# Kernel optimization log

Measured on AMD Instinct MI355X. Metric: run time of the kernel, lower is better.

Reference implementation:

```python
import jax, jax.numpy as jnp
import numpy as np

DIM = 512
H = 8
HD = DIM // H  # head_dim = 64


def setup_inputs() -> dict:
    key = jax.random.key(0)
    k1, k2, k3 = jax.random.split(key, 3)
    B, N = 16, 4096
    x = jax.random.normal(k1, (B, DIM, N), jnp.float32)
    # qkv_proj: Conv1d(dim, H*(1+2*HD), kernel=1) == linear over channels
    Wqkv = jax.random.normal(k2, (H * (1 + 2 * HD), DIM), jnp.float32) * 0.02
    bqkv = jnp.zeros((H * (1 + 2 * HD),), jnp.float32)
    # proj: Conv1d(dim, dim, kernel=1)
    Wp = jax.random.normal(k3, (DIM, DIM), jnp.float32) * 0.02
    bp = jnp.zeros((DIM,), jnp.float32)
    return {"x": x, "Wqkv": Wqkv, "bqkv": bqkv, "Wp": Wp, "bp": bp}


def reference(x, Wqkv, bqkv, Wp, bp):
    B, C, N = x.shape
    # 1x1 conv projection -> [B, H*(1+2*HD), N]
    qkv = jnp.einsum('oc,bcn->bon', Wqkv, x) + bqkv[None, :, None]
    qkv = qkv.reshape(B, H, 1 + 2 * HD, N)
    q = qkv[:, :, 0:1, :]          # [B,H,1,N]
    k = qkv[:, :, 1:1 + HD, :]     # [B,H,HD,N]
    v = qkv[:, :, 1 + HD:, :]      # [B,H,HD,N]
    scores = jax.nn.softmax(q, axis=-1)              # softmax over N
    ctx = jnp.sum(k * scores, axis=-1, keepdims=True)  # [B,H,HD,1]
    out = jax.nn.relu(v) * ctx                         # [B,H,HD,N]
    # permute/split/cat in torch == [B,H,HD,N] -> [B,N,H*HD] -> [B,C,N]
    out = out.transpose(0, 3, 1, 2).reshape(B, N, H * HD)
    out = out.transpose(0, 2, 1)                       # [B,C,N]
    out = jnp.einsum('oc,bcn->bon', Wp, out) + bp[None, :, None]
    return out
```

## Files before the change

### kernel.cpp

```cpp
#include <hip/hip_runtime.h>

#define NB 16
#define NC 512
#define NN 4096
#define NH 8

typedef __attribute__((ext_vector_type(8))) __bf16 bf16x8;
typedef __attribute__((ext_vector_type(4))) float f32x4;

__device__ __forceinline__ unsigned short f2bf(float f) {
    union { float f; unsigned u; } x; x.f = f;
    unsigned r = x.u + 0x7FFF + ((x.u >> 16) & 1);
    return (unsigned short)(r >> 16);
}

__global__ void pack_kernel(const float* __restrict__ Wqkv, const float* __restrict__ bqkv,
                            const float* __restrict__ Wp,
                            unsigned short* __restrict__ Wv_bf, unsigned short* __restrict__ Wp_bf,
                            float* __restrict__ bv) {
    int t = blockIdx.x * 256 + threadIdx.x;
    int j = t >> 9, c = t & 511;
    int h = j >> 6, d = j & 63;
    Wv_bf[t] = f2bf(Wqkv[((size_t)h * 129 + 65 + d) * 512 + c]);
    Wp_bf[t] = f2bf(Wp[t]);
    if (t < 512) bv[t] = bqkv[(t >> 6) * 129 + 65 + (t & 63)];
}

__global__ __launch_bounds__(256) void q_kernel(
        const float* __restrict__ x, const float* __restrict__ Wqkv,
        float* __restrict__ qP) {
    __shared__ float Ws[8][64];
    int n0 = blockIdx.x * 512, c0 = blockIdx.y * 64, b = blockIdx.z;
    int t = threadIdx.x;
    for (int i = t; i < 512; i += 256)
        Ws[i >> 6][i & 63] = Wqkv[(size_t)(i >> 6) * (129 * 512) + c0 + (i & 63)];
    __syncthreads();

    float acc[8][2];
#pragma unroll
    for (int h = 0; h < 8; h++) { acc[h][0] = 0.f; acc[h][1] = 0.f; }

    const float* xb = x + ((size_t)b * NC + c0) * NN + n0;
#pragma unroll 4
    for (int c = 0; c < 64; c++) {
        float2 v = *((const float2*)(xb + (size_t)c * NN) + t);
#pragma unroll
        for (int h = 0; h < 8; h++) {
            float w = Ws[h][c];
            acc[h][0] += w * v.x;
            acc[h][1] += w * v.y;
        }
    }
#pragma unroll
    for (int h = 0; h < 8; h++) {
        float2 o; o.x = acc[h][0]; o.y = acc[h][1];
        *((float2*)(qP + ((size_t)(blockIdx.y * NB + b) * 8 + h) * NN + n0) + t) = o;
    }
}

__global__ void softmax_kernel(const float* __restrict__ qP, float* __restrict__ sT) {
    int bh = blockIdx.x;
    int b = bh >> 3, h = bh & 7;
    int t = threadIdx.x;
    __shared__ float red[8];
    const float* qp = qP + (size_t)bh * NN;
    const size_t cstr = (size_t)NB * 8 * NN;
    float v[16];
    float mx = -1e30f;
#pragma unroll
    for (int i = 0; i < 16; i++) {
        int n = t + i * 256;
        float s = 0.f;
#pragma unroll
        for (int cb = 0; cb < 8; cb++) s += qp[cb * cstr + n];
        v[i] = s; mx = fmaxf(mx, s);
    }
#pragma unroll
    for (int o = 32; o; o >>= 1) mx = fmaxf(mx, __shfl_xor(mx, o));
    if ((t & 63) == 0) red[t >> 6] = mx;
    __syncthreads();
    mx = fmaxf(fmaxf(red[0], red[1]), fmaxf(red[2], red[3]));
    float s = 0.f;
#pragma unroll
    for (int i = 0; i < 16; i++) { v[i] = __expf(v[i] - mx); s += v[i]; }
#pragma unroll
    for (int o = 32; o; o >>= 1) s += __shfl_xor(s, o);
    __syncthreads();
    if ((t & 63) == 0) red[4 + (t >> 6)] = s;
    __syncthreads();
    float inv = 1.f / (red[4] + red[5] + red[6] + red[7]);
#pragma unroll
    for (int i = 0; i < 16; i++) {
        int n = t + i * 256;
        sT[((size_t)b * NN + n) * 8 + h] = v[i] * inv;
    }
}

__global__ __launch_bounds__(256) void xbar_kernel(
        const float* __restrict__ x, const float* __restrict__ sT,
        float* __restrict__ xbarP) {
    __shared__ float red[4][8][64];
    int c0 = blockIdx.x * 32, sl = blockIdx.y, b = blockIdx.z;
    int t = threadIdx.x;
    int l = t & 63, w = t >> 6;
    int nsl0 = sl * 512;
    float s_[8][8];
    {
        const f32x4* sp = (const f32x4*)(sT + ((size_t)b * NN + nsl0 + l * 8) * 8);
#pragma unroll
        for (int j = 0; j < 8; j++) {
            f32x4 a = sp[2 * j], bq = sp[2 * j + 1];
            s_[j][0] = a[0]; s_[j][1] = a[1]; s_[j][2] = a[2]; s_[j][3] = a[3];
            s_[j][4] = bq[0]; s_[j][5] = bq[1]; s_[j][6] = bq[2]; s_[j][7] = bq[3];
        }
    }
    float acc[8][8];
#pragma unroll
    for (int r = 0; r < 8; r++)
#pragma unroll
        for (int h = 0; h < 8; h++) acc[r][h] = 0.f;

    const float* xr = x + ((size_t)b * NC + c0 + w * 8) * NN + nsl0 + l * 8;
#pragma unroll
    for (int r = 0; r < 8; r++) {
        float4 a0 = *(const float4*)(xr + (size_t)r * NN);
        float4 a1 = *(const float4*)(xr + (size_t)r * NN + 4);
        float xf[8] = {a0.x, a0.y, a0.z, a0.w, a1.x, a1.y, a1.z, a1.w};
#pragma unroll
        for (int j = 0; j < 8; j++)
#pragma unroll
            for (int h = 0; h < 8; h++) acc[r][h] += xf[j] * s_[j][h];
    }
#pragma unroll
    for (int r = 0; r < 8; r++)
#pragma unroll
        for (int h = 0; h < 8; h++) {
            float a = acc[r][h];
            a += __shfl_xor(a, 8);
            a += __shfl_xor(a, 16);
            a += __shfl_xor(a, 32);
            acc[r][h] = a;
        }
    if (l < 8) {
#pragma unroll
        for (int r = 0; r < 8; r++)
#pragma unroll
            for (int h = 0; h < 8; h++) red[w][l][r * 8 + h] = acc[r][h];
    }
    __syncthreads();
    {
        int idx = t & 63;
        float v = 0.f;
#pragma unroll
        for (int res = 0; res < 8; res++) v += red[w][res][idx];
        int r = idx >> 3, h = idx & 7;
        xbarP[(((size_t)sl * NB + b) * 8 + h) * NC + c0 + w * 8 + r] = v;
    }
}

__global__ void ctx_kernel(const float* __restrict__ xbarP, const float* __restrict__ Wqkv,
                           const float* __restrict__ bqkv, float* __restrict__ ctx) {
    int bh = blockIdx.x; int b = bh >> 3, h = bh & 7;
    int t = threadIdx.x;
    __shared__ float xb[512];
    for (int i = t; i < 512; i += 256) {
        float s = 0.f;
#pragma unroll
        for (int sl = 0; sl < 8; sl++) s += xbarP[(((size_t)sl * NB + b) * 8 + h) * NC + i];
        xb[i] = s;
    }
    __syncthreads();
    int d = t >> 2, sub = t & 3;
    const float* wk = Wqkv + ((size_t)h * 129 + 1 + d) * 512;
    float acc = 0.f;
    for (int i = sub * 4; i < 512; i += 16) {
        float4 w = *(const float4*)(wk + i);
        acc += w.x * xb[i] + w.y * xb[i + 1] + w.z * xb[i + 2] + w.w * xb[i + 3];
    }
    acc += __shfl_xor(acc, 1);
    acc += __shfl_xor(acc, 2);
    if (sub == 0) ctx[(size_t)b * NC + h * 64 + d] = acc + bqkv[h * 129 + 1 + d];
}

__global__ __launch_bounds__(512, 2) void fused_gemm_kernel(
    const unsigned short* __restrict__ Wv,
    const unsigned short* __restrict__ Wp,
    const float* __restrict__ x,
    const float* __restrict__ bv,
    const float* __restrict__ bp,
    const float* __restrict__ ctx,
    float* __restrict__ outp)
{
    __shared__ alignas(16) unsigned short Ms[16 * 128 * 32];
    __shared__ alignas(16) unsigned short Bs[128 * 32];
    int b = blockIdx.y, n0 = blockIdx.x * 128;
    int t = threadIdx.x;
    int lane = t & 63, wid = t >> 6;
    int wj = wid >> 1, wn = wid & 1;
    int g = lane >> 4, col = lane & 15;
    int koff = g * 8;

    int sc = t >> 4, sn8 = (t & 15) * 8;

    f32x4 acc[8][4];
#pragma unroll
    for (int i = 0; i < 8; i++)
#pragma unroll
        for (int j = 0; j < 4; j++) { f32x4 z = {0.f, 0.f, 0.f, 0.f}; acc[i][j] = z; }

    bf16x8 afc[8], afn[8];
#pragma unroll
    for (int i = 0; i < 8; i++)
        afc[i] = *(const bf16x8*)(Wv + (size_t)(wj * 128 + i * 16 + col) * 512 + koff);

#pragma unroll 2
    for (int ks = 0; ks < 16; ks++) {
        int kk = ks * 32;
        {
            const float* xr = x + ((size_t)b * NC + kk + sc) * NN + n0 + sn8;
            float4 v0 = *(const float4*)(xr);
            float4 v1 = *(const float4*)(xr + 4);
            unsigned short xv[8] = {f2bf(v0.x), f2bf(v0.y), f2bf(v0.z), f2bf(v0.w),
                                    f2bf(v1.x), f2bf(v1.y), f2bf(v1.z), f2bf(v1.w)};
#pragma unroll
            for (int i = 0; i < 8; i++) {
                int nl = sn8 + i;
                int byte = nl * 64 + ((sc * 2) ^ (((nl >> 3) & 3) << 4));
                *(unsigned short*)((char*)Bs + byte) = xv[i];
            }
        }
        if (ks < 15) {
#pragma unroll
            for (int i = 0; i < 8; i++)
                afn[i] = *(const bf16x8*)(Wv + (size_t)(wj * 128 + i * 16 + col) * 512 + kk + 32 + koff);
        }
        __syncthreads();
        bf16x8 bfr[4];
#pragma unroll
        for (int j = 0; j < 4; j++) {
            int row = wn * 64 + j * 16 + col;
            int byte = row * 64 + ((koff * 2) ^ (((row >> 3) & 3) << 4));
            bfr[j] = *(const bf16x8*)((const char*)Bs + byte);
        }
#pragma unroll
        for (int i = 0; i < 8; i++)
#pragma unroll
            for (int j = 0; j < 4; j++)
                acc[i][j] = __builtin_amdgcn_mfma_f32_16x16x32_bf16(afc[i], bfr[j], acc[i][j], 0, 0, 0);
        __syncthreads();
#pragma unroll
        for (int i = 0; i < 8; i++) afc[i] = afn[i];
    }

#pragma unroll
    for (int i = 0; i < 8; i++) {
        int j0 = wj * 128 + i * 16 + g * 4;
        float4 bv4 = *(const float4*)(bv + j0);
        float4 cx4 = *(const float4*)(ctx + (size_t)b * NC + j0);
#pragma unroll
        for (int j = 0; j < 4; j++) {
            int n = wn * 64 + j * 16 + col;
            f32x4 a = acc[i][j];
            unsigned short h0 = f2bf(fmaxf(a[0] + bv4.x, 0.f) * cx4.x);
            unsigned short h1 = f2bf(fmaxf(a[1] + bv4.y, 0.f) * cx4.y);
            unsigned short h2 = f2bf(fmaxf(a[2] + bv4.z, 0.f) * cx4.z);
            unsigned short h3 = f2bf(fmaxf(a[3] + bv4.w, 0.f) * cx4.w);
            uint2 pk;
            pk.x = (unsigned)h0 | ((unsigned)h1 << 16);
            pk.y = (unsigned)h2 | ((unsigned)h3 << 16);
            *(uint2*)(Ms + (size_t)(j0 >> 5) * 4096 + n * 32 + (j0 & 31)) = pk;
        }
    }
    __syncthreads();

#pragma unroll
    for (int i = 0; i < 8; i++)
#pragma unroll
        for (int j = 0; j < 4; j++) { f32x4 z = {0.f, 0.f, 0.f, 0.f}; acc[i][j] = z; }
#pragma unroll
    for (int i = 0; i < 8; i++)
        afc[i] = *(const bf16x8*)(Wp + (size_t)(wj * 128 + i * 16 + col) * 512 + koff);

#pragma unroll 2
    for (int ks = 0; ks < 16; ks++) {
        int kk = ks * 32;
        if (ks < 15) {
#pragma unroll
            for (int i = 0; i < 8; i++)
                afn[i] = *(const bf16x8*)(Wp + (size_t)(wj * 128 + i * 16 + col) * 512 + kk + 32 + koff);
        }
        bf16x8 bfr[4];
#pragma unroll
        for (int j = 0; j < 4; j++)
            bfr[j] = *(const bf16x8*)(Ms + (size_t)ks * 4096 + (wn * 64 + j * 16 + col) * 32 + koff);
#pragma unroll
        for (int i = 0; i < 8; i++)
#pragma unroll
            for (int j = 0; j < 4; j++)
                acc[i][j] = __builtin_amdgcn_mfma_f32_16x16x32_bf16(afc[i], bfr[j], acc[i][j], 0, 0, 0);
#pragma unroll
        for (int i = 0; i < 8; i++) afc[i] = afn[i];
    }

#pragma unroll
    for (int i = 0; i < 8; i++) {
        int o0 = wj * 128 + i * 16 + g * 4;
        float4 bp4 = *(const float4*)(bp + o0);
#pragma unroll
        for (int j = 0; j < 4; j++) {
            int n = n0 + wn * 64 + j * 16 + col;
            f32x4 a = acc[i][j];
            float* op = outp + ((size_t)b * NC + o0) * NN + n;
            op[0]              = a[0] + bp4.x;
            op[NN]             = a[1] + bp4.y;
            op[2 * (size_t)NN] = a[2] + bp4.z;
            op[3 * (size_t)NN] = a[3] + bp4.w;
        }
    }
}

extern "C" void kernel_launch(void* const* d_in, const int* in_sizes, int n_in,
                              void* d_out, int out_size, void* d_ws, size_t ws_size,
                              hipStream_t stream) {
    const float* x    = (const float*)d_in[0];
    const float* Wqkv = (const float*)d_in[1];
    const float* bqkv = (const float*)d_in[2];
    const float* Wp   = (const float*)d_in[3];
    const float* bp   = (const float*)d_in[4];
    float* outp = (float*)d_out;

    char* ws = (char*)d_ws;
    float* sT    = (float*)(ws);
    float* qP    = (float*)(ws + 2097152);
    float* xbarP = (float*)(ws + 18874368);
    float* ctx   = (float*)(ws + 20971520);
    unsigned short* Wv_bf = (unsigned short*)(ws + 20971520 + 32768);
    unsigned short* Wp_bf = (unsigned short*)(ws + 20971520 + 32768 + 524288);
    float* bv    = (float*)(ws + 20971520 + 32768 + 1048576);

    pack_kernel<<<dim3(1024), 256, 0, stream>>>(Wqkv, bqkv, Wp, Wv_bf, Wp_bf, bv);
    q_kernel<<<dim3(8, 8, 16), 256, 0, stream>>>(x, Wqkv, qP);
    softmax_kernel<<<dim3(128), 256, 0, stream>>>(qP, sT);
    xbar_kernel<<<dim3(16, 8, 16), 256, 0, stream>>>(x, sT, xbarP);
    ctx_kernel<<<dim3(128), 256, 0, stream>>>(xbarP, Wqkv, bqkv, ctx);
    fused_gemm_kernel<<<dim3(32, 16), 512, 0, stream>>>(Wv_bf, Wp_bf, x, bv, bp, ctx, outp);
}
```

Baseline: 231.0 us.

## Halve fused GEMM N-tile, double-buffer x staging with K=64 steps

The fused V-projection/output-projection kernel now uses 64-column N tiles instead of 128, which doubles the grid to 1024 blocks and shrinks the intermediate LDS buffer (64 KB instead of 128 KB) so more blocks can be resident. x staging moves to a double-buffered, XOR-swizzled LDS layout with 64-wide K steps and register prefetch of the next slice, and weight fragments are loaded per iteration instead of software-prefetched. The intent is better occupancy and fewer barriers per K. The cost is twice the weight traffic per output element and possible load latency exposure with no weight prefetch.

```diff
diff --git a/kernel.cpp b/kernel.cpp
--- a/kernel.cpp
+++ b/kernel.cpp
@@ -191,65 +191,67 @@
     const float* __restrict__ ctx,
     float* __restrict__ outp)
 {
-    __shared__ alignas(16) unsigned short Ms[16 * 128 * 32];
-    __shared__ alignas(16) unsigned short Bs[128 * 32];
-    int b = blockIdx.y, n0 = blockIdx.x * 128;
+    __shared__ alignas(16) unsigned short Ms[8 * 64 * 64];
+    __shared__ alignas(16) unsigned short Xs[2][64 * 64];
+    int b = blockIdx.y, n0 = blockIdx.x * 64;
     int t = threadIdx.x;
     int lane = t & 63, wid = t >> 6;
     int wj = wid >> 1, wn = wid & 1;
     int g = lane >> 4, col = lane & 15;
-    int koff = g * 8;
-
-    int sc = t >> 4, sn8 = (t & 15) * 8;
-
-    f32x4 acc[8][4];
-#pragma unroll
-    for (int i = 0; i < 8; i++)
-#pragma unroll
-        for (int j = 0; j < 4; j++) { f32x4 z = {0.f, 0.f, 0.f, 0.f}; acc[i][j] = z; }
-
-    bf16x8 afc[8], afn[8];
-#pragma unroll
-    for (int i = 0; i < 8; i++)
-        afc[i] = *(const bf16x8*)(Wv + (size_t)(wj * 128 + i * 16 + col) * 512 + koff);
-
-#pragma unroll 2
-    for (int ks = 0; ks < 16; ks++) {
-        int kk = ks * 32;
+    int k8 = g * 8;
+
+    int cp = t >> 4, n4 = (t & 15) * 4;
+
+    f32x4 acc[8][2];
+#pragma unroll
+    for (int i = 0; i < 8; i++) { f32x4 z = {0.f,0.f,0.f,0.f}; acc[i][0] = z; acc[i][1] = z; }
+
+    float4 sv0, sv1;
+    {
+        const float* xr = x + ((size_t)b * NC + 2 * cp) * NN + n0 + n4;
+        sv0 = *(const float4*)(xr);
+        sv1 = *(const float4*)(xr + NN);
+    }
+
+    for (int k = 0; k < 8; k++) {
+        int kk = k * 64;
         {
-            const float* xr = x + ((size_t)b * NC + kk + sc) * NN + n0 + sn8;
-            float4 v0 = *(const float4*)(xr);
-            float4 v1 = *(const float4*)(xr + 4);
-            unsigned short xv[8] = {f2bf(v0.x), f2bf(v0.y), f2bf(v0.z), f2bf(v0.w),
-                                    f2bf(v1.x), f2bf(v1.y), f2bf(v1.z), f2bf(v1.w)};
-#pragma unroll
-            for (int i = 0; i < 8; i++) {
-                int nl = sn8 + i;
-                int byte = nl * 64 + ((sc * 2) ^ (((nl >> 3) & 3) << 4));
-                *(unsigned short*)((char*)Bs + byte) = xv[i];
+            unsigned short* base = Xs[k & 1];
+            unsigned w0 = (unsigned)f2bf(sv0.x) | ((unsigned)f2bf(sv1.x) << 16);
+            unsigned w1 = (unsigned)f2bf(sv0.y) | ((unsigned)f2bf(sv1.y) << 16);
+            unsigned w2 = (unsigned)f2bf(sv0.z) | ((unsigned)f2bf(sv1.z) << 16);
+            unsigned w3 = (unsigned)f2bf(sv0.w) | ((unsigned)f2bf(sv1.w) << 16);
+            *(unsigned*)((char*)base + (n4 + 0) * 128 + ((4 * cp) ^ (((n4 + 0) & 7) << 4))) = w0;
+            *(unsigned*)((char*)base + (n4 + 1) * 128 + ((4 * cp) ^ (((n4 + 1) & 7) << 4))) = w1;
+            *(unsigned*)((char*)base + (n4 + 2) * 128 + ((4 * cp) ^ (((n4 + 2) & 7) << 4))) = w2;
+            *(unsigned*)((char*)base + (n4 + 3) * 128 + ((4 * cp) ^ (((n4 + 3) & 7) << 4))) = w3;
+        }
+        __syncthreads();
+        if (k < 7) {
+            const float* xr = x + ((size_t)b * NC + kk + 64 + 2 * cp) * NN + n0 + n4;
+            sv0 = *(const float4*)(xr);
+            sv1 = *(const float4*)(xr + NN);
+        }
+        const char* xsb = (const char*)Xs[k & 1];
+        bf16x8 bfr[2][2];
+#pragma unroll
+        for (int n2 = 0; n2 < 2; n2++)
+#pragma unroll
+            for (int h = 0; h < 2; h++) {
+                int row = wn * 32 + n2 * 16 + col;
+                bfr[n2][h] = *(const bf16x8*)(xsb + row * 128 + ((2 * (h * 32 + k8)) ^ ((row & 7) << 4)));
             }
-        }
-        if (ks < 15) {
-#pragma unroll
-            for (int i = 0; i < 8; i++)
-                afn[i] = *(const bf16x8*)(Wv + (size_t)(wj * 128 + i * 16 + col) * 512 + kk + 32 + koff);
+#pragma unroll
+        for (int i = 0; i < 8; i++) {
+            const unsigned short* ar = Wv + (size_t)(wj * 128 + i * 16 + col) * 512 + kk + k8;
+            bf16x8 af0 = *(const bf16x8*)(ar);
+            bf16x8 af1 = *(const bf16x8*)(ar + 32);
+            acc[i][0] = __builtin_amdgcn_mfma_f32_16x16x32_bf16(af0, bfr[0][0], acc[i][0], 0, 0, 0);
+            acc[i][1] = __builtin_amdgcn_mfma_f32_16x16x32_bf16(af0, bfr[1][0], acc[i][1], 0, 0, 0);
+            acc[i][0] = __builtin_amdgcn_mfma_f32_16x16x32_bf16(af1, bfr[0][1], acc[i][0], 0, 0, 0);
+            acc[i][1] = __builtin_amdgcn_mfma_f32_16x16x32_bf16(af1, bfr[1][1], acc[i][1], 0, 0, 0);
         }
         __syncthreads();
-        bf16x8 bfr[4];
-#pragma unroll
-        for (int j = 0; j < 4; j++) {
-            int row = wn * 64 + j * 16 + col;
-            int byte = row * 64 + ((koff * 2) ^ (((row >> 3) & 3) << 4));
-            bfr[j] = *(const bf16x8*)((const char*)Bs + byte);
-        }
-#pragma unroll
-        for (int i = 0; i < 8; i++)
-#pragma unroll
-            for (int j = 0; j < 4; j++)
-                acc[i][j] = __builtin_amdgcn_mfma_f32_16x16x32_bf16(afc[i], bfr[j], acc[i][j], 0, 0, 0);
-        __syncthreads();
-#pragma unroll
-        for (int i = 0; i < 8; i++) afc[i] = afn[i];
     }
 
 #pragma unroll
@@ -258,9 +260,9 @@
         float4 bv4 = *(const float4*)(bv + j0);
         float4 cx4 = *(const float4*)(ctx + (size_t)b * NC + j0);
 #pragma unroll
-        for (int j = 0; j < 4; j++) {
-            int n = wn * 64 + j * 16 + col;
-            f32x4 a = acc[i][j];
+        for (int n2 = 0; n2 < 2; n2++) {
+            int n = wn * 32 + n2 * 16 + col;
+            f32x4 a = acc[i][n2];
             unsigned short h0 = f2bf(fmaxf(a[0] + bv4.x, 0.f) * cx4.x);
             unsigned short h1 = f2bf(fmaxf(a[1] + bv4.y, 0.f) * cx4.y);
             unsigned short h2 = f2bf(fmaxf(a[2] + bv4.z, 0.f) * cx4.z);
@@ -268,38 +270,36 @@
             uint2 pk;
             pk.x = (unsigned)h0 | ((unsigned)h1 << 16);
             pk.y = (unsigned)h2 | ((unsigned)h3 << 16);
-            *(uint2*)(Ms + (size_t)(j0 >> 5) * 4096 + n * 32 + (j0 & 31)) = pk;
-        }
-    }
-    __syncthreads();
-
-#pragma unroll
-    for (int i = 0; i < 8; i++)
-#pragma unroll
-        for (int j = 0; j < 4; j++) { f32x4 z = {0.f, 0.f, 0.f, 0.f}; acc[i][j] = z; }
-#pragma unroll
-    for (int i = 0; i < 8; i++)
-        afc[i] = *(const bf16x8*)(Wp + (size_t)(wj * 128 + i * 16 + col) * 512 + koff);
+            *(uint2*)((char*)Ms + (j0 >> 6) * 8192 + n * 128 + ((2 * (j0 & 63)) ^ ((n & 7) << 4))) = pk;
+        }
+    }
+    __syncthreads();
+
+#pragma unroll
+    for (int i = 0; i < 8; i++) { f32x4 z = {0.f,0.f,0.f,0.f}; acc[i][0] = z; acc[i][1] = z; }
 
 #pragma unroll 2
-    for (int ks = 0; ks < 16; ks++) {
-        int kk = ks * 32;
-        if (ks < 15) {
-#pragma unroll
-            for (int i = 0; i < 8; i++)
-                afn[i] = *(const bf16x8*)(Wp + (size_t)(wj * 128 + i * 16 + col) * 512 + kk + 32 + koff);
-        }
-        bf16x8 bfr[4];
-#pragma unroll
-        for (int j = 0; j < 4; j++)
-            bfr[j] = *(const bf16x8*)(Ms + (size_t)ks * 4096 + (wn * 64 + j * 16 + col) * 32 + koff);
-#pragma unroll
-        for (int i = 0; i < 8; i++)
-#pragma unroll
-            for (int j = 0; j < 4; j++)
-                acc[i][j] = __builtin_amdgcn_mfma_f32_16x16x32_bf16(afc[i], bfr[j], acc[i][j], 0, 0, 0);
-#pragma unroll
-        for (int i = 0; i < 8; i++) afc[i] = afn[i];
+    for (int k = 0; k < 8; k++) {
+        int kk = k * 64;
+        const char* msb = (const char*)Ms + k * 8192;
+        bf16x8 bfr[2][2];
+#pragma unroll
+        for (int n2 = 0; n2 < 2; n2++)
+#pragma unroll
+            for (int h = 0; h < 2; h++) {
+                int row = wn * 32 + n2 * 16 + col;
+                bfr[n2][h] = *(const bf16x8*)(msb + row * 128 + ((2 * (h * 32 + k8)) ^ ((row & 7) << 4)));
+            }
+#pragma unroll
+        for (int i = 0; i < 8; i++) {
+            const unsigned short* ar = Wp + (size_t)(wj * 128 + i * 16 + col) * 512 + kk + k8;
+            bf16x8 af0 = *(const bf16x8*)(ar);
+            bf16x8 af1 = *(const bf16x8*)(ar + 32);
+            acc[i][0] = __builtin_amdgcn_mfma_f32_16x16x32_bf16(af0, bfr[0][0], acc[i][0], 0, 0, 0);
+            acc[i][1] = __builtin_amdgcn_mfma_f32_16x16x32_bf16(af0, bfr[1][0], acc[i][1], 0, 0, 0);
+            acc[i][0] = __builtin_amdgcn_mfma_f32_16x16x32_bf16(af1, bfr[0][1], acc[i][0], 0, 0, 0);
+            acc[i][1] = __builtin_amdgcn_mfma_f32_16x16x32_bf16(af1, bfr[1][1], acc[i][1], 0, 0, 0);
+        }
     }
 
 #pragma unroll
@@ -307,9 +307,9 @@
         int o0 = wj * 128 + i * 16 + g * 4;
         float4 bp4 = *(const float4*)(bp + o0);
 #pragma unroll
-        for (int j = 0; j < 4; j++) {
-            int n = n0 + wn * 64 + j * 16 + col;
-            f32x4 a = acc[i][j];
+        for (int n2 = 0; n2 < 2; n2++) {
+            int n = n0 + wn * 32 + n2 * 16 + col;
+            f32x4 a = acc[i][n2];
             float* op = outp + ((size_t)b * NC + o0) * NN + n;
             op[0]              = a[0] + bp4.x;
             op[NN]             = a[1] + bp4.y;
@@ -343,5 +343,5 @@
     softmax_kernel<<<dim3(128), 256, 0, stream>>>(qP, sT);
     xbar_kernel<<<dim3(16, 8, 16), 256, 0, stream>>>(x, sT, xbarP);
     ctx_kernel<<<dim3(128), 256, 0, stream>>>(xbarP, Wqkv, bqkv, ctx);
-    fused_gemm_kernel<<<dim3(32, 16), 512, 0, stream>>>(Wv_bf, Wp_bf, x, bv, bp, ctx, outp);
-}
+    fused_gemm_kernel<<<dim3(64, 16), 512, 0, stream>>>(Wv_bf, Wp_bf, x, bv, bp, ctx, outp);
+}
```

New measurement: 354.4 us. 1.53x slower.
